# Performance work log

Hardware: AMD Instinct MI355X
Metric: run time of the kernel (lower is better)

## Reference

```python
import jax, jax.numpy as jnp
import numpy as np

N_NODES = 100000
LEAKY_SLOPE = 0.5


def setup_inputs() -> dict:
    key = jax.random.key(0)
    k1, k2, k3, k4, k5 = jax.random.split(key, 5)
    E, N, D = 1600000, N_NODES, 128
    row_idx = jax.random.randint(k1, (E,), 0, N, dtype=jnp.int32)
    col_idx = jax.random.randint(k2, (E,), 0, N, dtype=jnp.int32)
    adj_vals = jax.random.uniform(k3, (E,), dtype=jnp.float32)
    embeds = jax.random.normal(k4, (N, D), dtype=jnp.float32)
    zishiying = jax.random.normal(k5, (N, D), dtype=jnp.float32)
    return {"row_idx": row_idx, "col_idx": col_idx, "adj_vals": adj_vals,
            "embeds": embeds, "zishiying": zishiying}


def reference(row_idx, col_idx, adj_vals, embeds, zishiying):
    # aij = sigmoid(z) * 2 - 1  (elementwise gate in [-1, 1])
    gated = embeds * (jax.nn.sigmoid(zishiying) * 2.0 - 1.0)  # [N, D]
    # spmm(adj, gated): gather source-node features, scale by edge value,
    # scatter-add into destination nodes.
    msgs = adj_vals[:, None] * gated[col_idx]                 # [E, D]
    agg = jax.ops.segment_sum(msgs, row_idx, num_segments=N_NODES)  # [N, D]
    return jax.nn.leaky_relu(agg, negative_slope=LEAKY_SLOPE)
```

## Files before the change

kernel.cpp:

```cpp
#include <hip/hip_runtime.h>
#include <hip/hip_fp16.h>
#include <math.h>

#define DD 128
#define LEAKY 0.5f
#define RPB 128
#define RPB_SHIFT 7
#define MAXBIN 1024
#define CHUNK 2048
#define MAXBLK 1024
#define PACK_SHIFT 20


__global__ void gate_h_kernel(const float4* __restrict__ emb,
                              const float4* __restrict__ zs,
                              float4* __restrict__ gated_h, int n8) {
    int i = blockIdx.x * blockDim.x + threadIdx.x;
    int stride = gridDim.x * blockDim.x;
    for (; i < n8; i += stride) {
        float4 e0 = emb[2 * i], e1 = emb[2 * i + 1];
        float4 z0 = zs[2 * i], z1 = zs[2 * i + 1];
        float g0 = e0.x * (2.f / (1.f + __expf(-z0.x)) - 1.f);
        float g1 = e0.y * (2.f / (1.f + __expf(-z0.y)) - 1.f);
        float g2 = e0.z * (2.f / (1.f + __expf(-z0.z)) - 1.f);
        float g3 = e0.w * (2.f / (1.f + __expf(-z0.w)) - 1.f);
        float g4 = e1.x * (2.f / (1.f + __expf(-z1.x)) - 1.f);
        float g5 = e1.y * (2.f / (1.f + __expf(-z1.y)) - 1.f);
        float g6 = e1.z * (2.f / (1.f + __expf(-z1.z)) - 1.f);
        float g7 = e1.w * (2.f / (1.f + __expf(-z1.w)) - 1.f);
        union { __half2 h[4]; float4 f; } u;
        u.h[0] = __floats2half2_rn(g0, g1);
        u.h[1] = __floats2half2_rn(g2, g3);
        u.h[2] = __floats2half2_rn(g4, g5);
        u.h[3] = __floats2half2_rn(g6, g7);
        gated_h[i] = u.f;
    }
}


__global__ void hist_kernel(const int* __restrict__ row, int* __restrict__ ghist,
                            int E, int NBIN, int NBLK) {
    __shared__ int hist[MAXBIN];
    const int b = blockIdx.x;
    for (int i = threadIdx.x; i < NBIN; i += 256) hist[i] = 0;
    __syncthreads();
    const int base = b * CHUNK;
    #pragma unroll
    for (int it = 0; it < CHUNK / 256; ++it) {
        int e = base + it * 256 + threadIdx.x;
        if (e < E) atomicAdd(&hist[row[e] >> RPB_SHIFT], 1);
    }
    __syncthreads();
    for (int i = threadIdx.x; i < NBIN; i += 256)
        ghist[(size_t)i * NBLK + b] = hist[i];
}


__global__ void binscan_kernel(const int* __restrict__ ghist, int* __restrict__ gofs,
                               int* __restrict__ btot, int NBIN, int NBLK) {
    const int bin = blockIdx.x * 4 + (threadIdx.x >> 6);
    if (bin >= NBIN) return;
    const int lane = threadIdx.x & 63;
    const int* src = ghist + (size_t)bin * NBLK;
    int* dst = gofs + (size_t)bin * NBLK;
    int carry = 0;
    for (int k = 0; k < NBLK; k += 64) {
        int b = k + lane;
        int v = (b < NBLK) ? src[b] : 0;
        int x = v;
        #pragma unroll
        for (int off = 1; off < 64; off <<= 1) {
            int t = __shfl_up(x, off, 64);
            if (lane >= off) x += t;
        }
        if (b < NBLK) dst[b] = carry + x - v;
        carry += __shfl(x, 63, 64);
    }
    if (lane == 0) btot[bin] = carry;
}


__global__ void scan_kernel(const int* __restrict__ counts,
                            int* __restrict__ starts, int n) {
    __shared__ int wsum[16];
    __shared__ int wpre[16];
    __shared__ int total_s;
    __shared__ int carry_s;
    const int tid = threadIdx.x;
    const int lane = tid & 63;
    const int wid = tid >> 6;
    if (tid == 0) carry_s = 0;
    __syncthreads();
    for (int base = 0; base < n; base += 4096) {
        int i0 = base + tid * 4;
        int4 v = make_int4(0, 0, 0, 0);
        if (i0 + 0 < n) v.x = counts[i0 + 0];
        if (i0 + 1 < n) v.y = counts[i0 + 1];
        if (i0 + 2 < n) v.z = counts[i0 + 2];
        if (i0 + 3 < n) v.w = counts[i0 + 3];
        int s0 = v.x, s1 = s0 + v.y, s2 = s1 + v.z, s3 = s2 + v.w;
        int x = s3;
        #pragma unroll
        for (int off = 1; off < 64; off <<= 1) {
            int t = __shfl_up(x, off, 64);
            if (lane >= off) x += t;
        }
        if (lane == 63) wsum[wid] = x;
        __syncthreads();
        if (tid < 16) {
            int s = wsum[tid];
            #pragma unroll
            for (int off = 1; off < 16; off <<= 1) {
                int t = __shfl_up(s, off, 64);
                if (tid >= off) s += t;
            }
            wpre[tid] = s - wsum[tid];
            if (tid == 15) total_s = s;
        }
        __syncthreads();
        int pre = carry_s + wpre[wid] + (x - s3);
        if (i0 + 0 < n) starts[i0 + 0] = pre;
        if (i0 + 1 < n) starts[i0 + 1] = pre + s0;
        if (i0 + 2 < n) starts[i0 + 2] = pre + s1;
        if (i0 + 3 < n) starts[i0 + 3] = pre + s2;
        __syncthreads();
        if (tid == 0) carry_s += total_s;
        __syncthreads();
    }
    if (tid == 0) starts[n] = carry_s;
}


__global__ void scatter_sort_kernel(const int* __restrict__ row, const int* __restrict__ col,
                                    const float* __restrict__ val,
                                    const int* __restrict__ gofs, const int* __restrict__ bstart,
                                    int2* __restrict__ sorted, int E, int NBIN, int NBLK) {
    __shared__ int cur[MAXBIN];
    const int b = blockIdx.x;
    for (int i = threadIdx.x; i < NBIN; i += 256)
        cur[i] = bstart[i] + gofs[(size_t)i * NBLK + b];
    __syncthreads();
    const int base = b * CHUNK;
    #pragma unroll
    for (int it = 0; it < CHUNK / 256; ++it) {
        int e = base + it * 256 + threadIdx.x;
        if (e < E) {
            int r = row[e];
            int slot = atomicAdd(&cur[r >> RPB_SHIFT], 1);
            sorted[slot] = make_int2(col[e] | ((r & (RPB - 1)) << PACK_SHIFT),
                                     __float_as_int(val[e]));
        }
    }
}


__global__ void rowsort_kernel(const int2* __restrict__ sorted,
                               const int* __restrict__ bstart,
                               int2* __restrict__ csr,
                               int* __restrict__ rowstart, int N, int NBIN, int E) {
    __shared__ int cnt[RPB];
    __shared__ int cur[RPB];
    __shared__ int wsum[4];
    const int bin = blockIdx.x;
    const int tid = threadIdx.x;
    const int lane = tid & 63;
    const int wid = tid >> 6;
    for (int i = tid; i < RPB; i += 256) cnt[i] = 0;
    __syncthreads();
    const int beg = bstart[bin], end = bstart[bin + 1];
    for (int e = beg + tid; e < end; e += 256) {
        int rl = ((unsigned)sorted[e].x) >> PACK_SHIFT;
        atomicAdd(&cnt[rl], 1);
    }
    __syncthreads();
    int v = (tid < RPB) ? cnt[tid] : 0;
    int x = v;
    #pragma unroll
    for (int off = 1; off < 64; off <<= 1) {
        int t = __shfl_up(x, off, 64);
        if (lane >= off) x += t;
    }
    if (lane == 63) wsum[wid] = x;
    __syncthreads();
    int base = 0;
    #pragma unroll
    for (int w = 0; w < 4; ++w) if (w < wid) base += wsum[w];
    int excl = base + x - v;
    if (tid < RPB) {
        cur[tid] = beg + excl;
        int r = bin * RPB + tid;
        if (r < N) rowstart[r] = beg + excl;
    }
    if (tid == 0 && bin == 0) rowstart[N] = E;
    __syncthreads();
    for (int e = beg + tid; e < end; e += 256) {
        int2 cv = sorted[e];
        int rl = ((unsigned)cv.x) >> PACK_SHIFT;
        int slot = atomicAdd(&cur[rl], 1);
        csr[slot] = make_int2(cv.x & ((1 << PACK_SHIFT) - 1), cv.y);
    }
}


__global__ void gather_h_kernel(const int* __restrict__ starts,
                                const int2* __restrict__ csr,
                                const __half2* __restrict__ gated,
                                float* __restrict__ out, int N) {
    int gid = blockIdx.x * blockDim.x + threadIdx.x;
    int r = gid >> 6;
    if (r >= N) return;
    int lane = gid & 63;
    int beg = __builtin_amdgcn_readfirstlane(starts[r]);
    int end = __builtin_amdgcn_readfirstlane(starts[r + 1]);
    float2 acc = make_float2(0.f, 0.f);
    int j = beg;
    for (; j + 3 < end; j += 4) {
        int2 cv0 = csr[j];
        int2 cv1 = csr[j + 1];
        int2 cv2 = csr[j + 2];
        int2 cv3 = csr[j + 3];
        float2 g0 = __half22float2(gated[(size_t)cv0.x * 64 + lane]);
        float2 g1 = __half22float2(gated[(size_t)cv1.x * 64 + lane]);
        float2 g2 = __half22float2(gated[(size_t)cv2.x * 64 + lane]);
        float2 g3 = __half22float2(gated[(size_t)cv3.x * 64 + lane]);
        float v0 = __int_as_float(cv0.y);
        float v1 = __int_as_float(cv1.y);
        float v2 = __int_as_float(cv2.y);
        float v3 = __int_as_float(cv3.y);
        acc.x += v0 * g0.x; acc.y += v0 * g0.y;
        acc.x += v1 * g1.x; acc.y += v1 * g1.y;
        acc.x += v2 * g2.x; acc.y += v2 * g2.y;
        acc.x += v3 * g3.x; acc.y += v3 * g3.y;
    }
    for (; j < end; ++j) {
        int2 cv = csr[j];
        float2 g = __half22float2(gated[(size_t)cv.x * 64 + lane]);
        float v = __int_as_float(cv.y);
        acc.x += v * g.x; acc.y += v * g.y;
    }
    acc.x = acc.x > 0.f ? acc.x : LEAKY * acc.x;
    acc.y = acc.y > 0.f ? acc.y : LEAKY * acc.y;
    ((float2*)out)[(size_t)r * 64 + lane] = acc;
}


__global__ void zero4_kernel(float4* __restrict__ out, int n4) {
    int i = blockIdx.x * blockDim.x + threadIdx.x;
    int stride = gridDim.x * blockDim.x;
    float4 z = make_float4(0.f, 0.f, 0.f, 0.f);
    for (; i < n4; i += stride) out[i] = z;
}

__global__ void scatter_fused_kernel(const int* __restrict__ row,
                                     const int* __restrict__ col,
                                     const float* __restrict__ val,
                                     const float* __restrict__ emb,
                                     const float* __restrict__ zs,
                                     float* __restrict__ out, int E) {
    int gid = blockIdx.x * blockDim.x + threadIdx.x;
    int e = gid >> 5;
    if (e >= E) return;
    int lane = gid & 31;
    int r = row[e];
    int c = col[e];
    float v = val[e];
    const float4* ep = (const float4*)(emb + (size_t)c * DD);
    const float4* zp = (const float4*)(zs + (size_t)c * DD);
    float4 ev = ep[lane];
    float4 zv = zp[lane];
    float4 gv;
    gv.x = ev.x * (2.f / (1.f + __expf(-zv.x)) - 1.f);
    gv.y = ev.y * (2.f / (1.f + __expf(-zv.y)) - 1.f);
    gv.z = ev.z * (2.f / (1.f + __expf(-zv.z)) - 1.f);
    gv.w = ev.w * (2.f / (1.f + __expf(-zv.w)) - 1.f);
    float* o = out + (size_t)r * DD + lane * 4;
    atomicAdd(o + 0, v * gv.x);
    atomicAdd(o + 1, v * gv.y);
    atomicAdd(o + 2, v * gv.z);
    atomicAdd(o + 3, v * gv.w);
}

__global__ void leaky_kernel(float4* __restrict__ out, int n4) {
    int i = blockIdx.x * blockDim.x + threadIdx.x;
    int stride = gridDim.x * blockDim.x;
    for (; i < n4; i += stride) {
        float4 x = out[i];
        x.x = x.x > 0.f ? x.x : LEAKY * x.x;
        x.y = x.y > 0.f ? x.y : LEAKY * x.y;
        x.z = x.z > 0.f ? x.z : LEAKY * x.z;
        x.w = x.w > 0.f ? x.w : LEAKY * x.w;
        out[i] = x;
    }
}


extern "C" void kernel_launch(void* const* d_in, const int* in_sizes, int n_in,
                              void* d_out, int out_size, void* d_ws, size_t ws_size,
                              hipStream_t stream) {
    const int* row_idx = (const int*)d_in[0];
    const int* col_idx = (const int*)d_in[1];
    const float* adj_vals = (const float*)d_in[2];
    const float* embeds = (const float*)d_in[3];
    const float* zishiying = (const float*)d_in[4];
    float* out = (float*)d_out;

    const int E = in_sizes[0];
    const int ND = in_sizes[3];
    const int N = ND / DD;
    const int n4 = ND / 4;
    const int n8 = ND / 8;
    const int NBIN = (N + RPB - 1) / RPB;
    const int NBLK = (E + CHUNK - 1) / CHUNK;

    char* p = (char*)d_ws;
    __half2* gated = (__half2*)p;          p += (size_t)ND * 2;
    int* ghist = (int*)p;                  p += (size_t)NBIN * NBLK * 4;
    int* gofs = (int*)p;                   p += (size_t)NBIN * NBLK * 4;
    int* btot = (int*)p;                   p += (size_t)NBIN * 4;
    int* bstart = (int*)p;                 p += (size_t)(NBIN + 1) * 4;
    int* rowstart = (int*)p;               p += (size_t)(N + 1) * 4;
    p = (char*)(((uintptr_t)p + 15) & ~(uintptr_t)15);
    int2* sorted = (int2*)p;               p += (size_t)E * 8;
    int2* csr = (int2*)p;                  p += (size_t)E * 8;
    const size_t need = (size_t)(p - (char*)d_ws);

    const int gb8 = min((n8 + 255) / 256, 2048);

    const bool ok = (NBIN <= MAXBIN) && (NBLK <= MAXBLK) && (N <= (1 << PACK_SHIFT)) &&
                    (ws_size >= need);

    if (ok) {
        hipLaunchKernelGGL(gate_h_kernel, dim3(gb8), dim3(256), 0, stream,
                           (const float4*)embeds, (const float4*)zishiying,
                           (float4*)gated, n8);
        hipLaunchKernelGGL(hist_kernel, dim3(NBLK), dim3(256), 0, stream,
                           row_idx, ghist, E, NBIN, NBLK);
        hipLaunchKernelGGL(binscan_kernel, dim3((NBIN + 3) / 4), dim3(256), 0, stream,
                           ghist, gofs, btot, NBIN, NBLK);
        hipLaunchKernelGGL(scan_kernel, dim3(1), dim3(1024), 0, stream,
                           btot, bstart, NBIN);
        hipLaunchKernelGGL(scatter_sort_kernel, dim3(NBLK), dim3(256), 0, stream,
                           row_idx, col_idx, adj_vals, gofs, bstart, sorted, E, NBIN, NBLK);
        hipLaunchKernelGGL(rowsort_kernel, dim3(NBIN), dim3(256), 0, stream,
                           sorted, bstart, csr, rowstart, N, NBIN, E);
        long long total = (long long)N * 64;
        int blocks = (int)((total + 255) / 256);
        hipLaunchKernelGGL(gather_h_kernel, dim3(blocks), dim3(256), 0, stream,
                           rowstart, csr, gated, out, N);
        return;
    }

    const int gb = min((n4 + 255) / 256, 2048);
    hipLaunchKernelGGL(zero4_kernel, dim3(gb), dim3(256), 0, stream, (float4*)out, n4);
    {
        long long total = (long long)E * 32;
        int sblocks = (int)((total + 255) / 256);
        hipLaunchKernelGGL(scatter_fused_kernel, dim3(sblocks), dim3(256), 0, stream,
                           row_idx, col_idx, adj_vals, embeds, zishiying, out, E);
    }
    hipLaunchKernelGGL(leaky_kernel, dim3(gb), dim3(256), 0, stream, (float4*)out, n4);
}
```

Measured before the change: 144.3 us.

## Fuse gate with histogram, transpose bin-histogram layout, drop single-block scan kernel

Merges the gating kernel and the per-chunk row-bin histogram into one launch, and stores the histogram block-major so the scatter kernel reads its offsets contiguously. The single-block global scan over bin totals is removed: each scatter block and each rowsort block recomputes the exclusive scan of the ~782 bin totals in shared memory. This cuts two kernel launches and a serial one-block kernel at the cost of redundant per-block scans and strided reads in the bin-scan kernel.

```diff
diff --git a/kernel.cpp b/kernel.cpp
--- a/kernel.cpp
+++ b/kernel.cpp
@@ -12,9 +12,26 @@
 #define PACK_SHIFT 20
 
 
-__global__ void gate_h_kernel(const float4* __restrict__ emb,
-                              const float4* __restrict__ zs,
-                              float4* __restrict__ gated_h, int n8) {
+__global__ void gatehist_kernel(const float4* __restrict__ emb,
+                                const float4* __restrict__ zs,
+                                float4* __restrict__ gated_h, int n8,
+                                const int* __restrict__ row, int* __restrict__ ghistT,
+                                int E, int NBIN, int NBLK) {
+    __shared__ int hist[MAXBIN];
+    const int b = blockIdx.x;
+    if (b < NBLK) {
+        for (int i = threadIdx.x; i < NBIN; i += 256) hist[i] = 0;
+        __syncthreads();
+        const int base = b * CHUNK;
+        #pragma unroll
+        for (int it = 0; it < CHUNK / 256; ++it) {
+            int e = base + it * 256 + threadIdx.x;
+            if (e < E) atomicAdd(&hist[row[e] >> RPB_SHIFT], 1);
+        }
+        __syncthreads();
+        for (int i = threadIdx.x; i < NBIN; i += 256)
+            ghistT[(size_t)b * NBIN + i] = hist[i];
+    }
     int i = blockIdx.x * blockDim.x + threadIdx.x;
     int stride = gridDim.x * blockDim.x;
     for (; i < n8; i += stride) {
@@ -38,136 +55,121 @@
 }
 
 
-__global__ void hist_kernel(const int* __restrict__ row, int* __restrict__ ghist,
-                            int E, int NBIN, int NBLK) {
-    __shared__ int hist[MAXBIN];
-    const int b = blockIdx.x;
-    for (int i = threadIdx.x; i < NBIN; i += 256) hist[i] = 0;
-    __syncthreads();
-    const int base = b * CHUNK;
-    #pragma unroll
-    for (int it = 0; it < CHUNK / 256; ++it) {
-        int e = base + it * 256 + threadIdx.x;
-        if (e < E) atomicAdd(&hist[row[e] >> RPB_SHIFT], 1);
-    }
-    __syncthreads();
-    for (int i = threadIdx.x; i < NBIN; i += 256)
-        ghist[(size_t)i * NBLK + b] = hist[i];
-}
-
-
-__global__ void binscan_kernel(const int* __restrict__ ghist, int* __restrict__ gofs,
-                               int* __restrict__ btot, int NBIN, int NBLK) {
+__global__ void binscanT_kernel(const int* __restrict__ ghistT, int* __restrict__ gofsT,
+                                int* __restrict__ btot, int NBIN, int NBLK) {
     const int bin = blockIdx.x * 4 + (threadIdx.x >> 6);
     if (bin >= NBIN) return;
     const int lane = threadIdx.x & 63;
-    const int* src = ghist + (size_t)bin * NBLK;
-    int* dst = gofs + (size_t)bin * NBLK;
     int carry = 0;
     for (int k = 0; k < NBLK; k += 64) {
         int b = k + lane;
-        int v = (b < NBLK) ? src[b] : 0;
+        int v = (b < NBLK) ? ghistT[(size_t)b * NBIN + bin] : 0;
         int x = v;
         #pragma unroll
         for (int off = 1; off < 64; off <<= 1) {
             int t = __shfl_up(x, off, 64);
             if (lane >= off) x += t;
         }
-        if (b < NBLK) dst[b] = carry + x - v;
+        if (b < NBLK) gofsT[(size_t)b * NBIN + bin] = carry + x - v;
         carry += __shfl(x, 63, 64);
     }
     if (lane == 0) btot[bin] = carry;
 }
 
 
-__global__ void scan_kernel(const int* __restrict__ counts,
-                            int* __restrict__ starts, int n) {
-    __shared__ int wsum[16];
-    __shared__ int wpre[16];
-    __shared__ int total_s;
-    __shared__ int carry_s;
+__global__ void scatter_sortT_kernel(const int* __restrict__ row, const int* __restrict__ col,
+                                     const float* __restrict__ val,
+                                     const int* __restrict__ gofsT, const int* __restrict__ btot,
+                                     int2* __restrict__ sorted, int E, int NBIN, int NBLK) {
+    __shared__ int cur[MAXBIN];
+    __shared__ int wsum[4];
+    const int b = blockIdx.x;
     const int tid = threadIdx.x;
     const int lane = tid & 63;
     const int wid = tid >> 6;
-    if (tid == 0) carry_s = 0;
-    __syncthreads();
-    for (int base = 0; base < n; base += 4096) {
-        int i0 = base + tid * 4;
-        int4 v = make_int4(0, 0, 0, 0);
-        if (i0 + 0 < n) v.x = counts[i0 + 0];
-        if (i0 + 1 < n) v.y = counts[i0 + 1];
-        if (i0 + 2 < n) v.z = counts[i0 + 2];
-        if (i0 + 3 < n) v.w = counts[i0 + 3];
-        int s0 = v.x, s1 = s0 + v.y, s2 = s1 + v.z, s3 = s2 + v.w;
+    for (int i = tid; i < NBIN; i += 256) cur[i] = btot[i];
+    __syncthreads();
+    int i0 = tid * 4;
+    int c0 = (i0 + 0 < NBIN) ? cur[i0 + 0] : 0;
+    int c1 = (i0 + 1 < NBIN) ? cur[i0 + 1] : 0;
+    int c2 = (i0 + 2 < NBIN) ? cur[i0 + 2] : 0;
+    int c3 = (i0 + 3 < NBIN) ? cur[i0 + 3] : 0;
+    int s0 = c0, s1 = s0 + c1, s2 = s1 + c2, s3 = s2 + c3;
+    int x = s3;
+    #pragma unroll
+    for (int off = 1; off < 64; off <<= 1) {
+        int t = __shfl_up(x, off, 64);
+        if (lane >= off) x += t;
+    }
+    if (lane == 63) wsum[wid] = x;
+    __syncthreads();
+    int base = 0;
+    #pragma unroll
+    for (int w = 0; w < 4; ++w) if (w < wid) base += wsum[w];
+    int excl = base + x - s3;
+    const size_t gbase = (size_t)b * NBIN;
+    if (i0 + 0 < NBIN) cur[i0 + 0] = excl + gofsT[gbase + i0 + 0];
+    if (i0 + 1 < NBIN) cur[i0 + 1] = excl + s0 + gofsT[gbase + i0 + 1];
+    if (i0 + 2 < NBIN) cur[i0 + 2] = excl + s1 + gofsT[gbase + i0 + 2];
+    if (i0 + 3 < NBIN) cur[i0 + 3] = excl + s2 + gofsT[gbase + i0 + 3];
+    __syncthreads();
+    const int ebase = b * CHUNK;
+    #pragma unroll
+    for (int it = 0; it < CHUNK / 256; ++it) {
+        int e = ebase + it * 256 + tid;
+        if (e < E) {
+            int r = row[e];
+            int slot = atomicAdd(&cur[r >> RPB_SHIFT], 1);
+            sorted[slot] = make_int2(col[e] | ((r & (RPB - 1)) << PACK_SHIFT),
+                                     __float_as_int(val[e]));
+        }
+    }
+}
+
+
+__global__ void rowsortT_kernel(const int2* __restrict__ sorted,
+                                const int* __restrict__ btot,
+                                int2* __restrict__ csr,
+                                int* __restrict__ rowstart, int N, int NBIN, int E) {
+    __shared__ int bs[MAXBIN + 1];
+    __shared__ int wsA[4];
+    __shared__ int cnt[RPB];
+    __shared__ int cur[RPB];
+    __shared__ int wsB[4];
+    const int bin = blockIdx.x;
+    const int tid = threadIdx.x;
+    const int lane = tid & 63;
+    const int wid = tid >> 6;
+    for (int i = tid; i < NBIN; i += 256) bs[i] = btot[i];
+    __syncthreads();
+    {
+        int i0 = tid * 4;
+        int c0 = (i0 + 0 < NBIN) ? bs[i0 + 0] : 0;
+        int c1 = (i0 + 1 < NBIN) ? bs[i0 + 1] : 0;
+        int c2 = (i0 + 2 < NBIN) ? bs[i0 + 2] : 0;
+        int c3 = (i0 + 3 < NBIN) ? bs[i0 + 3] : 0;
+        int s0 = c0, s1 = s0 + c1, s2 = s1 + c2, s3 = s2 + c3;
         int x = s3;
         #pragma unroll
         for (int off = 1; off < 64; off <<= 1) {
             int t = __shfl_up(x, off, 64);
             if (lane >= off) x += t;
         }
-        if (lane == 63) wsum[wid] = x;
+        if (lane == 63) wsA[wid] = x;
         __syncthreads();
-        if (tid < 16) {
-            int s = wsum[tid];
-            #pragma unroll
-            for (int off = 1; off < 16; off <<= 1) {
-                int t = __shfl_up(s, off, 64);
-                if (tid >= off) s += t;
-            }
-            wpre[tid] = s - wsum[tid];
-            if (tid == 15) total_s = s;
-        }
-        __syncthreads();
-        int pre = carry_s + wpre[wid] + (x - s3);
-        if (i0 + 0 < n) starts[i0 + 0] = pre;
-        if (i0 + 1 < n) starts[i0 + 1] = pre + s0;
-        if (i0 + 2 < n) starts[i0 + 2] = pre + s1;
-        if (i0 + 3 < n) starts[i0 + 3] = pre + s2;
-        __syncthreads();
-        if (tid == 0) carry_s += total_s;
-        __syncthreads();
-    }
-    if (tid == 0) starts[n] = carry_s;
-}
-
-
-__global__ void scatter_sort_kernel(const int* __restrict__ row, const int* __restrict__ col,
-                                    const float* __restrict__ val,
-                                    const int* __restrict__ gofs, const int* __restrict__ bstart,
-                                    int2* __restrict__ sorted, int E, int NBIN, int NBLK) {
-    __shared__ int cur[MAXBIN];
-    const int b = blockIdx.x;
-    for (int i = threadIdx.x; i < NBIN; i += 256)
-        cur[i] = bstart[i] + gofs[(size_t)i * NBLK + b];
-    __syncthreads();
-    const int base = b * CHUNK;
-    #pragma unroll
-    for (int it = 0; it < CHUNK / 256; ++it) {
-        int e = base + it * 256 + threadIdx.x;
-        if (e < E) {
-            int r = row[e];
-            int slot = atomicAdd(&cur[r >> RPB_SHIFT], 1);
-            sorted[slot] = make_int2(col[e] | ((r & (RPB - 1)) << PACK_SHIFT),
-                                     __float_as_int(val[e]));
-        }
-    }
-}
-
-
-__global__ void rowsort_kernel(const int2* __restrict__ sorted,
-                               const int* __restrict__ bstart,
-                               int2* __restrict__ csr,
-                               int* __restrict__ rowstart, int N, int NBIN, int E) {
-    __shared__ int cnt[RPB];
-    __shared__ int cur[RPB];
-    __shared__ int wsum[4];
-    const int bin = blockIdx.x;
-    const int tid = threadIdx.x;
-    const int lane = tid & 63;
-    const int wid = tid >> 6;
+        int base = 0;
+        #pragma unroll
+        for (int w = 0; w < 4; ++w) if (w < wid) base += wsA[w];
+        int excl = base + x - s3;
+        if (i0 + 0 < NBIN) bs[i0 + 0] = excl;
+        if (i0 + 1 < NBIN) bs[i0 + 1] = excl + s0;
+        if (i0 + 2 < NBIN) bs[i0 + 2] = excl + s1;
+        if (i0 + 3 < NBIN) bs[i0 + 3] = excl + s2;
+        if (tid == 0) bs[NBIN] = E;
+    }
     for (int i = tid; i < RPB; i += 256) cnt[i] = 0;
     __syncthreads();
-    const int beg = bstart[bin], end = bstart[bin + 1];
+    const int beg = bs[bin], end = bs[bin + 1];
     for (int e = beg + tid; e < end; e += 256) {
         int rl = ((unsigned)sorted[e].x) >> PACK_SHIFT;
         atomicAdd(&cnt[rl], 1);
@@ -180,11 +182,11 @@
         int t = __shfl_up(x, off, 64);
         if (lane >= off) x += t;
     }
-    if (lane == 63) wsum[wid] = x;
+    if (lane == 63) wsB[wid] = x;
     __syncthreads();
     int base = 0;
     #pragma unroll
-    for (int w = 0; w < 4; ++w) if (w < wid) base += wsum[w];
+    for (int w = 0; w < 4; ++w) if (w < wid) base += wsB[w];
     int excl = base + x - v;
     if (tid < RPB) {
         cur[tid] = beg + excl;
@@ -314,10 +316,9 @@
 
     char* p = (char*)d_ws;
     __half2* gated = (__half2*)p;          p += (size_t)ND * 2;
-    int* ghist = (int*)p;                  p += (size_t)NBIN * NBLK * 4;
-    int* gofs = (int*)p;                   p += (size_t)NBIN * NBLK * 4;
+    int* ghistT = (int*)p;                 p += (size_t)NBIN * NBLK * 4;
+    int* gofsT = (int*)p;                  p += (size_t)NBIN * NBLK * 4;
     int* btot = (int*)p;                   p += (size_t)NBIN * 4;
-    int* bstart = (int*)p;                 p += (size_t)(NBIN + 1) * 4;
     int* rowstart = (int*)p;               p += (size_t)(N + 1) * 4;
     p = (char*)(((uintptr_t)p + 15) & ~(uintptr_t)15);
     int2* sorted = (int2*)p;               p += (size_t)E * 8;
@@ -330,19 +331,16 @@
                     (ws_size >= need);
 
     if (ok) {
-        hipLaunchKernelGGL(gate_h_kernel, dim3(gb8), dim3(256), 0, stream,
+        int fused_grid = max(NBLK, gb8);
+        hipLaunchKernelGGL(gatehist_kernel, dim3(fused_grid), dim3(256), 0, stream,
                            (const float4*)embeds, (const float4*)zishiying,
-                           (float4*)gated, n8);
-        hipLaunchKernelGGL(hist_kernel, dim3(NBLK), dim3(256), 0, stream,
-                           row_idx, ghist, E, NBIN, NBLK);
-        hipLaunchKernelGGL(binscan_kernel, dim3((NBIN + 3) / 4), dim3(256), 0, stream,
-                           ghist, gofs, btot, NBIN, NBLK);
-        hipLaunchKernelGGL(scan_kernel, dim3(1), dim3(1024), 0, stream,
-                           btot, bstart, NBIN);
-        hipLaunchKernelGGL(scatter_sort_kernel, dim3(NBLK), dim3(256), 0, stream,
-                           row_idx, col_idx, adj_vals, gofs, bstart, sorted, E, NBIN, NBLK);
-        hipLaunchKernelGGL(rowsort_kernel, dim3(NBIN), dim3(256), 0, stream,
-                           sorted, bstart, csr, rowstart, N, NBIN, E);
+                           (float4*)gated, n8, row_idx, ghistT, E, NBIN, NBLK);
+        hipLaunchKernelGGL(binscanT_kernel, dim3((NBIN + 3) / 4), dim3(256), 0, stream,
+                           ghistT, gofsT, btot, NBIN, NBLK);
+        hipLaunchKernelGGL(scatter_sortT_kernel, dim3(NBLK), dim3(256), 0, stream,
+                           row_idx, col_idx, adj_vals, gofsT, btot, sorted, E, NBIN, NBLK);
+        hipLaunchKernelGGL(rowsortT_kernel, dim3(NBIN), dim3(256), 0, stream,
+                           sorted, btot, csr, rowstart, N, NBIN, E);
         long long total = (long long)N * 64;
         int blocks = (int)((total + 255) / 256);
         hipLaunchKernelGGL(gather_h_kernel, dim3(blocks), dim3(256), 0, stream,
```

Result: faster. 136.4 us (-5.5%).
